# Performance work log

Hardware: AMD Instinct MI355X
Metric: run time of the kernel (lower is better)

## Reference

```python
import jax, jax.numpy as jnp
import numpy as np

Z_RES, N_RES = 128, 512
M_PTS = 2_000_000


def trilinear_devoxelize(grid, coords):
    """Gather-based trilinear interpolation.
    grid:   (Z, N, N, C) voxel grid
    coords: (M, 3) float positions in voxel index space (z, x, y)
    returns (M, C)
    """
    Zd, Nd = grid.shape[0], grid.shape[1]
    c0f = jnp.floor(coords)
    frac = coords - c0f                      # (M, 3) fractional offsets
    maxi = jnp.array([Zd - 1, Nd - 1, Nd - 1], dtype=jnp.int32)
    c0 = jnp.clip(c0f.astype(jnp.int32), 0, maxi)
    c1 = jnp.clip(c0 + 1, 0, maxi)
    fz, fx, fy = frac[:, 0:1], frac[:, 1:2], frac[:, 2:3]
    gz, gx, gy = 1.0 - fz, 1.0 - fx, 1.0 - fy

    def g(zi, xi, yi):
        return grid[zi, xi, yi]              # (M, C) gather

    out = (g(c0[:, 0], c0[:, 1], c0[:, 2]) * gz * gx * gy
         + g(c0[:, 0], c0[:, 1], c1[:, 2]) * gz * gx * fy
         + g(c0[:, 0], c1[:, 1], c0[:, 2]) * gz * fx * gy
         + g(c0[:, 0], c1[:, 1], c1[:, 2]) * gz * fx * fy
         + g(c1[:, 0], c0[:, 1], c0[:, 2]) * fz * gx * gy
         + g(c1[:, 0], c0[:, 1], c1[:, 2]) * fz * gx * fy
         + g(c1[:, 0], c1[:, 1], c0[:, 2]) * fz * fx * gy
         + g(c1[:, 0], c1[:, 1], c1[:, 2]) * fz * fx * fy)
    return out


def setup_inputs() -> dict:
    key = jax.random.key(0)
    k1, k2 = jax.random.split(key)
    extents = jnp.array([Z_RES - 1, N_RES - 1, N_RES - 1], jnp.float32)
    coords = jax.random.uniform(k1, (M_PTS, 3), dtype=jnp.float32) * extents
    # init_scale = 1.0 -> albedo ~ U[0,1); normal initialized to zeros (per module)
    albedo = jax.random.uniform(k2, (Z_RES, N_RES, N_RES), dtype=jnp.float32)
    normal = jnp.zeros((Z_RES, N_RES, N_RES, 3), dtype=jnp.float32)
    return {"coords": coords, "albedo": albedo, "normal": normal}


def reference(coords, albedo, normal):
    base_normal = jnp.array([-1.0, 0.0, 0.0], dtype=jnp.float32)
    a = trilinear_devoxelize(albedo[..., None], coords)[:, 0]   # (M,)
    n = trilinear_devoxelize(normal, coords)                    # (M, 3)
    a = jax.nn.elu(a)
    n = jnp.tanh(n) + base_normal
    # F.normalize(dim=1, eps=1e-12): divide by max(||n||, eps)
    norm = jnp.maximum(jnp.linalg.norm(n, axis=1, keepdims=True), 1e-12)
    n = n / norm
    return (a, n)
```

## Files before the change

### kernel.cpp

```cpp
#include <hip/hip_runtime.h>
#include <math.h>

#define ZR 128
#define NR 512
#define ZB1 4096

typedef unsigned int u32x4 __attribute__((ext_vector_type(4)));
typedef unsigned short u16x8 __attribute__((ext_vector_type(8)));
typedef unsigned long long u64x2v __attribute__((ext_vector_type(2)));


__device__ __forceinline__ float bf16_to_f32(unsigned short u) {
    return __uint_as_float(((unsigned int)u) << 16);
}

__device__ __forceinline__ unsigned short f32_to_bf16_rne(float v) {
    unsigned int u = __float_as_uint(v);
    return (unsigned short)((u + 0x7FFFu + ((u >> 16) & 1u)) >> 16);
}

__device__ __forceinline__ float extract_bf16(u64x2v v, int yo) {
    unsigned long long w = (yo & 4) ? v.y : v.x;
    unsigned int sh = ((unsigned)yo & 3u) << 4;
    return bf16_to_f32((unsigned short)(w >> sh));
}

__device__ __forceinline__ void zcheck_range(
    const u32x4* __restrict__ normal4, long long lo, long long hi,
    long long rank, long long nthreads, unsigned int* __restrict__ flag)
{
    unsigned int acc = 0;
    long long i = lo + rank * 256 + threadIdx.x;
    for (; i + nthreads < hi; i += 2 * nthreads) {
        u32x4 v0 = __builtin_nontemporal_load(&normal4[i]);
        u32x4 v1 = __builtin_nontemporal_load(&normal4[i + nthreads]);
        acc |= v0.x | v0.y | v0.z | v0.w | v1.x | v1.y | v1.z | v1.w;
    }
    if (i < hi) {
        u32x4 v = __builtin_nontemporal_load(&normal4[i]);
        acc |= v.x | v.y | v.z | v.w;
    }
    if (__ballot(acc != 0) && ((threadIdx.x & 63) == 0))
        atomicOr(flag, 1u);
}

__device__ __forceinline__ float interp_rows(
    const unsigned short* __restrict__ tiled,
    float cz, float cx, float cy)
{
    float fz0 = floorf(cz), fx0 = floorf(cx), fy0 = floorf(cy);
    float fz = cz - fz0, fx = cx - fx0, fy = cy - fy0;

    int z0 = min(max((int)fz0, 0), ZR - 1);
    int x0 = min(max((int)fx0, 0), NR - 1);
    int y0 = min(max((int)fy0, 0), NR - 1);
    int z1 = min(z0 + 1, ZR - 1);
    int x1 = min(x0 + 1, NR - 1);
    int y1 = min(y0 + 1, NR - 1);

    float gz = 1.0f - fz, gx = 1.0f - fx, gy = 1.0f - fy;

    float w000 = gz * gx * gy, w001 = gz * gx * fy;
    float w010 = gz * fx * gy, w011 = gz * fx * fy;
    float w100 = fz * gx * gy, w101 = fz * gx * fy;
    float w110 = fz * fx * gy, w111 = fz * fx * fy;

    int xo0 = (x0 & 3) << 3, xo1 = (x1 & 3) << 3;
    int yo0 = y0 & 7,        yo1 = y1 & 7;
    int c0 = (y0 >> 3) << 5, c1 = (y1 >> 3) << 5;
    int r00 = ((z0 << 7) + (x0 >> 2)) << 11;
    int r01 = ((z0 << 7) + (x1 >> 2)) << 11;
    int r10 = ((z1 << 7) + (x0 >> 2)) << 11;
    int r11 = ((z1 << 7) + (x1 >> 2)) << 11;

    const u64x2v* base = (const u64x2v*)tiled;

    u64x2v vA = base[(r00 + c0 + xo0) >> 3];
    u64x2v vB = base[(r01 + c0 + xo1) >> 3];
    u64x2v vC = base[(r10 + c0 + xo0) >> 3];
    u64x2v vD = base[(r11 + c0 + xo1) >> 3];

    u64x2v vA2 = vA, vB2 = vB, vC2 = vC, vD2 = vD;
    if (c1 != c0) {
        vA2 = base[(r00 + c1 + xo0) >> 3];
        vB2 = base[(r01 + c1 + xo1) >> 3];
        vC2 = base[(r10 + c1 + xo0) >> 3];
        vD2 = base[(r11 + c1 + xo1) >> 3];
    }

    return
        extract_bf16(vA,  yo0) * w000 + extract_bf16(vA2, yo1) * w001 +
        extract_bf16(vB,  yo0) * w010 + extract_bf16(vB2, yo1) * w011 +
        extract_bf16(vC,  yo0) * w100 + extract_bf16(vC2, yo1) * w101 +
        extract_bf16(vD,  yo0) * w110 + extract_bf16(vD2, yo1) * w111;
}

__global__ __launch_bounds__(256) void phase1_kernel(
    const float* __restrict__ albedo,
    unsigned short* __restrict__ tiled,
    const u32x4* __restrict__ normal4,
    const unsigned int* __restrict__ normal_tail, int tail_cnt,
    unsigned int* __restrict__ flag,
    float* __restrict__ out_n,
    long long n4, int M, int FB)
{
    unsigned int b = blockIdx.x;

    if (b < (unsigned)ZB1) {
        if (b == 0 && threadIdx.x < (unsigned)tail_cnt) {
            if (normal_tail[threadIdx.x]) atomicOr(flag, 1u);
        }
        zcheck_range(normal4, 0, n4, (long long)b, (long long)ZB1 * 256, flag);
        return;
    }
    b -= (unsigned)ZB1;

    if (b < 16384u) {
        int z = (int)(b >> 7);
        int xt = (int)(b & 127u);

        __shared__ float s[2048];
        const u32x4* src = (const u32x4*)(albedo + ((size_t)z * NR + (size_t)xt * 4) * NR);
        for (int k = threadIdx.x; k < 512; k += 256) {
            u32x4 v = __builtin_nontemporal_load(&src[k]);
            ((u32x4*)s)[k] = v;
        }
        __syncthreads();

        unsigned short* dst = tiled + (size_t)b * 2048;
        int t8 = threadIdx.x * 8;
        u16x8 outv;
#pragma unroll
        for (int j = 0; j < 8; j++) {
            int k = t8 + j;
            int yt = k >> 5;
            int r = k & 31;
            int xr = r >> 3;
            int yy = r & 7;
            outv[j] = f32_to_bf16_rne(s[xr * 512 + (yt << 3) + yy]);
        }
        *(u16x8*)(dst + t8) = outv;
        return;
    }
    b -= 16384u;

    long long total = 3LL * M;
    if ((M & 3) == 0) {
        long long f4 = (long long)b * 256 + threadIdx.x;
        long long nf4 = total >> 2;
        if (f4 < nf4) {
            const unsigned int B = 0xBF800000u;
            int rmod = (int)(f4 % 3);
            u32x4 v;
            if (rmod == 0)      v = (u32x4){B, 0u, 0u, B};
            else if (rmod == 1) v = (u32x4){0u, 0u, B, 0u};
            else                v = (u32x4){0u, B, 0u, 0u};
            __builtin_nontemporal_store(v, &((u32x4*)out_n)[f4]);
        }
    } else {
        long long stride = (long long)FB * 256;
        for (long long qq = (long long)b * 256 + threadIdx.x; qq < total; qq += stride)
            out_n[qq] = ((qq % 3) == 0) ? -1.0f : 0.0f;
    }
}

__global__ __launch_bounds__(256) void interp_kernel(
    const float* __restrict__ coords,
    const unsigned short* __restrict__ tiled,
    float* __restrict__ out_a,
    int M)
{
    int i = blockIdx.x * 256 + threadIdx.x;
    if (i >= M) return;

    float cz = coords[3 * i + 0];
    float cx = coords[3 * i + 1];
    float cy = coords[3 * i + 2];

    float a = interp_rows(tiled, cz, cx, cy);
    a = (a > 0.0f) ? a : expm1f(a);
    __builtin_nontemporal_store(a, &out_a[i]);
}

__global__ __launch_bounds__(256) void normal_full_kernel(
    const float* __restrict__ coords,
    const float* __restrict__ normal,
    const unsigned int* __restrict__ flag,
    float* __restrict__ out_n,
    int M)
{
    if (*flag == 0) return;

    int stride = gridDim.x * 256;
    for (int i = blockIdx.x * 256 + threadIdx.x; i < M; i += stride) {
        float cz = coords[3 * i + 0];
        float cx = coords[3 * i + 1];
        float cy = coords[3 * i + 2];

        float fz0 = floorf(cz), fx0 = floorf(cx), fy0 = floorf(cy);
        float fz = cz - fz0, fx = cx - fx0, fy = cy - fy0;

        int z0 = min(max((int)fz0, 0), ZR - 1);
        int x0 = min(max((int)fx0, 0), NR - 1);
        int y0 = min(max((int)fy0, 0), NR - 1);
        int z1 = min(z0 + 1, ZR - 1);
        int x1 = min(x0 + 1, NR - 1);
        int y1 = min(y0 + 1, NR - 1);

        float gz = 1.0f - fz, gx = 1.0f - fx, gy = 1.0f - fy;

        float w000 = gz * gx * gy, w001 = gz * gx * fy;
        float w010 = gz * fx * gy, w011 = gz * fx * fy;
        float w100 = fz * gx * gy, w101 = fz * gx * fy;
        float w110 = fz * fx * gy, w111 = fz * fx * fy;

        size_t b00 = ((size_t)z0 * NR + x0) * NR;
        size_t b01 = ((size_t)z0 * NR + x1) * NR;
        size_t b10 = ((size_t)z1 * NR + x0) * NR;
        size_t b11 = ((size_t)z1 * NR + x1) * NR;

        float n0 = 0.0f, n1 = 0.0f, n2 = 0.0f;
#define ACC(base, yy, w)                                           \
        {                                                          \
            const float* qp = normal + ((base) + (size_t)(yy)) * 3;\
            n0 += qp[0] * (w);                                     \
            n1 += qp[1] * (w);                                     \
            n2 += qp[2] * (w);                                     \
        }
        ACC(b00, y0, w000); ACC(b00, y1, w001);
        ACC(b01, y0, w010); ACC(b01, y1, w011);
        ACC(b10, y0, w100); ACC(b10, y1, w101);
        ACC(b11, y0, w110); ACC(b11, y1, w111);
#undef ACC

        n0 = tanhf(n0) - 1.0f;
        n1 = tanhf(n1);
        n2 = tanhf(n2);

        float nrm = sqrtf(n0 * n0 + n1 * n1 + n2 * n2);
        nrm = fmaxf(nrm, 1e-12f);
        float inv = 1.0f / nrm;

        out_n[3 * i + 0] = n0 * inv;
        out_n[3 * i + 1] = n1 * inv;
        out_n[3 * i + 2] = n2 * inv;
    }
}

__global__ __launch_bounds__(256) void devox_direct(
    const float* __restrict__ coords,
    const float* __restrict__ albedo,
    const float* __restrict__ normal,
    float* __restrict__ out_a,
    float* __restrict__ out_n,
    int M)
{
    int i = blockIdx.x * 256 + threadIdx.x;
    if (i >= M) return;

    float cz = coords[3 * i + 0];
    float cx = coords[3 * i + 1];
    float cy = coords[3 * i + 2];

    float fz0 = floorf(cz), fx0 = floorf(cx), fy0 = floorf(cy);
    float fz = cz - fz0, fx = cx - fx0, fy = cy - fy0;

    int z0 = min(max((int)fz0, 0), ZR - 1);
    int x0 = min(max((int)fx0, 0), NR - 1);
    int y0 = min(max((int)fy0, 0), NR - 1);
    int z1 = min(z0 + 1, ZR - 1);
    int x1 = min(x0 + 1, NR - 1);
    int y1 = min(y0 + 1, NR - 1);

    float gz = 1.0f - fz, gx = 1.0f - fx, gy = 1.0f - fy;
    float w000 = gz * gx * gy, w001 = gz * gx * fy;
    float w010 = gz * fx * gy, w011 = gz * fx * fy;
    float w100 = fz * gx * gy, w101 = fz * gx * fy;
    float w110 = fz * fx * gy, w111 = fz * fx * fy;

    size_t b00 = ((size_t)z0 * NR + x0) * NR;
    size_t b01 = ((size_t)z0 * NR + x1) * NR;
    size_t b10 = ((size_t)z1 * NR + x0) * NR;
    size_t b11 = ((size_t)z1 * NR + x1) * NR;

    float a =
        albedo[b00 + y0] * w000 + albedo[b00 + y1] * w001 +
        albedo[b01 + y0] * w010 + albedo[b01 + y1] * w011 +
        albedo[b10 + y0] * w100 + albedo[b10 + y1] * w101 +
        albedo[b11 + y0] * w110 + albedo[b11 + y1] * w111;

    float n0 = 0.0f, n1 = 0.0f, n2 = 0.0f;
#define ACC(base, yy, w)                                           \
    {                                                              \
        const float* qp = normal + ((base) + (size_t)(yy)) * 3;    \
        n0 += qp[0] * (w);                                         \
        n1 += qp[1] * (w);                                         \
        n2 += qp[2] * (w);                                         \
    }
    ACC(b00, y0, w000); ACC(b00, y1, w001);
    ACC(b01, y0, w010); ACC(b01, y1, w011);
    ACC(b10, y0, w100); ACC(b10, y1, w101);
    ACC(b11, y0, w110); ACC(b11, y1, w111);
#undef ACC

    a = (a > 0.0f) ? a : expm1f(a);
    n0 = tanhf(n0) - 1.0f;
    n1 = tanhf(n1);
    n2 = tanhf(n2);
    float nrm = sqrtf(n0 * n0 + n1 * n1 + n2 * n2);
    nrm = fmaxf(nrm, 1e-12f);
    float inv = 1.0f / nrm;

    out_a[i] = a;
    out_n[3 * i + 0] = n0 * inv;
    out_n[3 * i + 1] = n1 * inv;
    out_n[3 * i + 2] = n2 * inv;
}

extern "C" void kernel_launch(void* const* d_in, const int* in_sizes, int n_in,
                              void* d_out, int out_size, void* d_ws, size_t ws_size,
                              hipStream_t stream) {
    const float* coords = (const float*)d_in[0];
    const float* albedo = (const float*)d_in[1];
    const float* normal = (const float*)d_in[2];

    int M = in_sizes[0] / 3;
    long long normal_elems = (long long)in_sizes[2];
    long long n4 = normal_elems / 4;
    int tail_cnt = (int)(normal_elems & 3);
    const unsigned int* normal_tail = (const unsigned int*)normal + n4 * 4;

    float* out = (float*)d_out;
    float* out_a = out;
    float* out_n = out + M;

    size_t tiled_off = 256;
    size_t tiled_bytes = (size_t)128 * 128 * 64 * 32 * 2;
    if (ws_size < tiled_off + tiled_bytes) {
        int nblk = (M + 255) / 256;
        devox_direct<<<nblk, 256, 0, stream>>>(coords, albedo, normal, out_a, out_n, M);
        return;
    }

    unsigned int* flag = (unsigned int*)d_ws;
    unsigned short* tiled = (unsigned short*)((char*)d_ws + tiled_off);

    (void)hipMemsetAsync(flag, 0, sizeof(unsigned int), stream);

    long long total_n = 3LL * M;
    int FB = ((M & 3) == 0) ? (int)((total_n / 4 + 255) / 256) : 2048;
    if (FB < 1) FB = 1;
    phase1_kernel<<<ZB1 + 16384 + FB, 256, 0, stream>>>(
        albedo, tiled, (const u32x4*)normal, normal_tail, tail_cnt,
        flag, out_n, n4, M, FB);

    int iblk = (M + 255) / 256;
    interp_kernel<<<iblk, 256, 0, stream>>>(coords, tiled, out_a, M);

    normal_full_kernel<<<2048, 256, 0, stream>>>(coords, normal, flag, out_n, M);
}
```

Baseline: 681.8 us.

## Move normal zero-check into interp kernel and process two points per thread

The zero-scan of the normal grid moves out of the repack kernel and into the interpolation kernel, where every third block does zero-check work and the other two do interpolation. Mixing them lets the bandwidth-heavy scan overlap with the latency-bound gathers. Each interpolation thread now handles two points, using float2 coordinate loads and a paired output store. The risk is uneven block mixes and a different zcheck grid size changing scan efficiency.

```diff
diff --git a/kernel.cpp b/kernel.cpp
--- a/kernel.cpp
+++ b/kernel.cpp
@@ -3,11 +3,11 @@
 
 #define ZR 128
 #define NR 512
-#define ZB1 4096
 
 typedef unsigned int u32x4 __attribute__((ext_vector_type(4)));
 typedef unsigned short u16x8 __attribute__((ext_vector_type(8)));
 typedef unsigned long long u64x2v __attribute__((ext_vector_type(2)));
+typedef float f32x2 __attribute__((ext_vector_type(2)));
 
 
 __device__ __forceinline__ float bf16_to_f32(unsigned short u) {
@@ -95,25 +95,13 @@
         extract_bf16(vD,  yo0) * w110 + extract_bf16(vD2, yo1) * w111;
 }
 
-__global__ __launch_bounds__(256) void phase1_kernel(
+__global__ __launch_bounds__(256) void repack_fill_kernel(
     const float* __restrict__ albedo,
     unsigned short* __restrict__ tiled,
-    const u32x4* __restrict__ normal4,
-    const unsigned int* __restrict__ normal_tail, int tail_cnt,
-    unsigned int* __restrict__ flag,
     float* __restrict__ out_n,
-    long long n4, int M, int FB)
+    int M, int FB)
 {
     unsigned int b = blockIdx.x;
-
-    if (b < (unsigned)ZB1) {
-        if (b == 0 && threadIdx.x < (unsigned)tail_cnt) {
-            if (normal_tail[threadIdx.x]) atomicOr(flag, 1u);
-        }
-        zcheck_range(normal4, 0, n4, (long long)b, (long long)ZB1 * 256, flag);
-        return;
-    }
-    b -= (unsigned)ZB1;
 
     if (b < 16384u) {
         int z = (int)(b >> 7);
@@ -164,22 +152,46 @@
     }
 }
 
-__global__ __launch_bounds__(256) void interp_kernel(
+__global__ __launch_bounds__(256) void interp_zcheck_kernel(
     const float* __restrict__ coords,
     const unsigned short* __restrict__ tiled,
+    const u32x4* __restrict__ normal4,
+    const unsigned int* __restrict__ normal_tail, int tail_cnt,
+    unsigned int* __restrict__ flag,
     float* __restrict__ out_a,
-    int M)
-{
-    int i = blockIdx.x * 256 + threadIdx.x;
-    if (i >= M) return;
-
-    float cz = coords[3 * i + 0];
-    float cx = coords[3 * i + 1];
-    float cy = coords[3 * i + 2];
-
-    float a = interp_rows(tiled, cz, cx, cy);
-    a = (a > 0.0f) ? a : expm1f(a);
-    __builtin_nontemporal_store(a, &out_a[i]);
+    int M, long long n4, int ZB)
+{
+    unsigned int b = blockIdx.x;
+    unsigned int q = b / 3u;
+    unsigned int r = b - 3u * q;
+
+    if (r == 2u) {
+        if (q == 0 && threadIdx.x < (unsigned)tail_cnt) {
+            if (normal_tail[threadIdx.x]) atomicOr(flag, 1u);
+        }
+        zcheck_range(normal4, 0, n4, (long long)q, (long long)ZB * 256, flag);
+        return;
+    }
+
+    int ib = (int)(2u * q + r);
+    int t = ib * 256 + (int)threadIdx.x;
+    int i0 = t * 2;
+    if (i0 >= M) return;
+
+    const float2* cp = (const float2*)(coords + (size_t)i0 * 3);
+    float2 q0 = cp[0], q1 = cp[1], q2 = cp[2];
+
+    float a0 = interp_rows(tiled, q0.x, q0.y, q1.x);
+    a0 = (a0 > 0.0f) ? a0 : expm1f(a0);
+
+    if (i0 + 1 < M) {
+        float a1 = interp_rows(tiled, q1.y, q2.x, q2.y);
+        a1 = (a1 > 0.0f) ? a1 : expm1f(a1);
+        f32x2 av; av.x = a0; av.y = a1;
+        __builtin_nontemporal_store(av, (f32x2*)(out_a + i0));
+    } else {
+        out_a[i0] = a0;
+    }
 }
 
 __global__ __launch_bounds__(256) void normal_full_kernel(
@@ -350,12 +362,15 @@
     long long total_n = 3LL * M;
     int FB = ((M & 3) == 0) ? (int)((total_n / 4 + 255) / 256) : 2048;
     if (FB < 1) FB = 1;
-    phase1_kernel<<<ZB1 + 16384 + FB, 256, 0, stream>>>(
-        albedo, tiled, (const u32x4*)normal, normal_tail, tail_cnt,
-        flag, out_n, n4, M, FB);
-
-    int iblk = (M + 255) / 256;
-    interp_kernel<<<iblk, 256, 0, stream>>>(coords, tiled, out_a, M);
+    repack_fill_kernel<<<16384 + FB, 256, 0, stream>>>(albedo, tiled, out_n, M, FB);
+
+    int IB = (M + 511) / 512;
+    IB = (IB + 1) & ~1;
+    if (IB < 2) IB = 2;
+    int ZB = IB / 2;
+    interp_zcheck_kernel<<<3 * ZB, 256, 0, stream>>>(
+        coords, tiled, (const u32x4*)normal, normal_tail, tail_cnt,
+        flag, out_a, M, n4, ZB);
 
     normal_full_kernel<<<2048, 256, 0, stream>>>(coords, normal, flag, out_n, M);
 }
```

After: 674.5 us. About the same (-1.1%).

## Bin points into spatial cells and interpolate from shared-memory albedo tiles

Applied to the files above, without the earlier changes.

Replaces the bf16 retiling of the whole albedo grid plus per-point global gathers with a scatter pass that buckets points by spatial cell (4x32x32 voxels) using atomics. A per-cell kernel then loads a small albedo halo tile into LDS and interpolates every point in the bucket from shared memory, writing output by original index. Points beyond the per-cell capacity go to an overflow list handled by a separate global-gather kernel. This removes the full-grid bf16 conversion pass and the precision loss, at the cost of atomic contention, scattered output writes and an extra record write/read of the points.

```diff
diff --git a/kernel.cpp b/kernel.cpp
--- a/kernel.cpp
+++ b/kernel.cpp
@@ -3,27 +3,17 @@
 
 #define ZR 128
 #define NR 512
-#define ZB1 4096
+
+#define NCX 16
+#define NCY 16
+#define NCELL 8192
+#define CAP 512
+#define SLZ 5
+#define SLX 33
+#define SLY 33
+#define SVOL (SLZ * SLX * SLY)
 
 typedef unsigned int u32x4 __attribute__((ext_vector_type(4)));
-typedef unsigned short u16x8 __attribute__((ext_vector_type(8)));
-typedef unsigned long long u64x2v __attribute__((ext_vector_type(2)));
-
-
-__device__ __forceinline__ float bf16_to_f32(unsigned short u) {
-    return __uint_as_float(((unsigned int)u) << 16);
-}
-
-__device__ __forceinline__ unsigned short f32_to_bf16_rne(float v) {
-    unsigned int u = __float_as_uint(v);
-    return (unsigned short)((u + 0x7FFFu + ((u >> 16) & 1u)) >> 16);
-}
-
-__device__ __forceinline__ float extract_bf16(u64x2v v, int yo) {
-    unsigned long long w = (yo & 4) ? v.y : v.x;
-    unsigned int sh = ((unsigned)yo & 3u) << 4;
-    return bf16_to_f32((unsigned short)(w >> sh));
-}
 
 __device__ __forceinline__ void zcheck_range(
     const u32x4* __restrict__ normal4, long long lo, long long hi,
@@ -44,105 +34,54 @@
         atomicOr(flag, 1u);
 }
 
-__device__ __forceinline__ float interp_rows(
-    const unsigned short* __restrict__ tiled,
-    float cz, float cx, float cy)
-{
-    float fz0 = floorf(cz), fx0 = floorf(cx), fy0 = floorf(cy);
-    float fz = cz - fz0, fx = cx - fx0, fy = cy - fy0;
-
-    int z0 = min(max((int)fz0, 0), ZR - 1);
-    int x0 = min(max((int)fx0, 0), NR - 1);
-    int y0 = min(max((int)fy0, 0), NR - 1);
-    int z1 = min(z0 + 1, ZR - 1);
-    int x1 = min(x0 + 1, NR - 1);
-    int y1 = min(y0 + 1, NR - 1);
-
-    float gz = 1.0f - fz, gx = 1.0f - fx, gy = 1.0f - fy;
-
-    float w000 = gz * gx * gy, w001 = gz * gx * fy;
-    float w010 = gz * fx * gy, w011 = gz * fx * fy;
-    float w100 = fz * gx * gy, w101 = fz * gx * fy;
-    float w110 = fz * fx * gy, w111 = fz * fx * fy;
-
-    int xo0 = (x0 & 3) << 3, xo1 = (x1 & 3) << 3;
-    int yo0 = y0 & 7,        yo1 = y1 & 7;
-    int c0 = (y0 >> 3) << 5, c1 = (y1 >> 3) << 5;
-    int r00 = ((z0 << 7) + (x0 >> 2)) << 11;
-    int r01 = ((z0 << 7) + (x1 >> 2)) << 11;
-    int r10 = ((z1 << 7) + (x0 >> 2)) << 11;
-    int r11 = ((z1 << 7) + (x1 >> 2)) << 11;
-
-    const u64x2v* base = (const u64x2v*)tiled;
-
-    u64x2v vA = base[(r00 + c0 + xo0) >> 3];
-    u64x2v vB = base[(r01 + c0 + xo1) >> 3];
-    u64x2v vC = base[(r10 + c0 + xo0) >> 3];
-    u64x2v vD = base[(r11 + c0 + xo1) >> 3];
-
-    u64x2v vA2 = vA, vB2 = vB, vC2 = vC, vD2 = vD;
-    if (c1 != c0) {
-        vA2 = base[(r00 + c1 + xo0) >> 3];
-        vB2 = base[(r01 + c1 + xo1) >> 3];
-        vC2 = base[(r10 + c1 + xo0) >> 3];
-        vD2 = base[(r11 + c1 + xo1) >> 3];
-    }
-
-    return
-        extract_bf16(vA,  yo0) * w000 + extract_bf16(vA2, yo1) * w001 +
-        extract_bf16(vB,  yo0) * w010 + extract_bf16(vB2, yo1) * w011 +
-        extract_bf16(vC,  yo0) * w100 + extract_bf16(vC2, yo1) * w101 +
-        extract_bf16(vD,  yo0) * w110 + extract_bf16(vD2, yo1) * w111;
-}
-
-__global__ __launch_bounds__(256) void phase1_kernel(
-    const float* __restrict__ albedo,
-    unsigned short* __restrict__ tiled,
+__global__ __launch_bounds__(256) void scatter_zcheck_fill_kernel(
+    const float* __restrict__ coords,
     const u32x4* __restrict__ normal4,
     const unsigned int* __restrict__ normal_tail, int tail_cnt,
     unsigned int* __restrict__ flag,
+    unsigned int* __restrict__ cnt,
+    unsigned int* __restrict__ ovf_cnt,
+    float4* __restrict__ recs,
+    float4* __restrict__ ovf,
     float* __restrict__ out_n,
-    long long n4, int M, int FB)
+    int M, long long n4, int SB, int ZB, int FB)
 {
     unsigned int b = blockIdx.x;
 
-    if (b < (unsigned)ZB1) {
+    if (b < (unsigned)SB) {
+        int base = (int)b * 2048;
+#pragma unroll
+        for (int k = 0; k < 8; k++) {
+            int i = base + k * 256 + (int)threadIdx.x;
+            if (i >= M) break;
+            size_t o = 3 * (size_t)i;
+            float cz = coords[o], cx = coords[o + 1], cy = coords[o + 2];
+            int z0 = min(max((int)floorf(cz), 0), ZR - 1);
+            int x0 = min(max((int)floorf(cx), 0), NR - 1);
+            int y0 = min(max((int)floorf(cy), 0), NR - 1);
+            int cell = ((z0 >> 2) * NCX + (x0 >> 5)) * NCY + (y0 >> 5);
+            unsigned int slot = atomicAdd(&cnt[cell], 1u);
+            float4 r;
+            r.x = cz; r.y = cx; r.z = cy; r.w = __uint_as_float((unsigned int)i);
+            if (slot < CAP) {
+                recs[(size_t)cell * CAP + slot] = r;
+            } else {
+                unsigned int os = atomicAdd(ovf_cnt, 1u);
+                ovf[os] = r;
+            }
+        }
+        return;
+    }
+    b -= (unsigned)SB;
+
+    if (b < (unsigned)ZB) {
         if (b == 0 && threadIdx.x < (unsigned)tail_cnt) {
             if (normal_tail[threadIdx.x]) atomicOr(flag, 1u);
         }
-        zcheck_range(normal4, 0, n4, (long long)b, (long long)ZB1 * 256, flag);
+        zcheck_range(normal4, 0, n4, (long long)b, (long long)ZB * 256, flag);
         return;
     }
-    b -= (unsigned)ZB1;
-
-    if (b < 16384u) {
-        int z = (int)(b >> 7);
-        int xt = (int)(b & 127u);
-
-        __shared__ float s[2048];
-        const u32x4* src = (const u32x4*)(albedo + ((size_t)z * NR + (size_t)xt * 4) * NR);
-        for (int k = threadIdx.x; k < 512; k += 256) {
-            u32x4 v = __builtin_nontemporal_load(&src[k]);
-            ((u32x4*)s)[k] = v;
-        }
-        __syncthreads();
-
-        unsigned short* dst = tiled + (size_t)b * 2048;
-        int t8 = threadIdx.x * 8;
-        u16x8 outv;
-#pragma unroll
-        for (int j = 0; j < 8; j++) {
-            int k = t8 + j;
-            int yt = k >> 5;
-            int r = k & 31;
-            int xr = r >> 3;
-            int yy = r & 7;
-            outv[j] = f32_to_bf16_rne(s[xr * 512 + (yt << 3) + yy]);
-        }
-        *(u16x8*)(dst + t8) = outv;
-        return;
-    }
-    b -= 16384u;
+    b -= (unsigned)ZB;
 
     long long total = 3LL * M;
     if ((M & 3) == 0) {
@@ -164,22 +103,116 @@
     }
 }
 
-__global__ __launch_bounds__(256) void interp_kernel(
-    const float* __restrict__ coords,
-    const unsigned short* __restrict__ tiled,
+__global__ __launch_bounds__(256) void interp_cell_kernel(
+    const float* __restrict__ albedo,
+    const unsigned int* __restrict__ cnt,
+    const float4* __restrict__ recs,
+    float* __restrict__ out_a)
+{
+    __shared__ float s[SVOL];
+
+    int c = blockIdx.x;
+    int zc = c >> 8;
+    int xc = (c >> 4) & 15;
+    int yc = c & 15;
+    int Z = zc << 2, X = xc << 5, Y = yc << 5;
+
+    for (int i = threadIdx.x; i < SVOL; i += 256) {
+        int lz = i / (SLX * SLY);
+        int rem = i - lz * (SLX * SLY);
+        int lx = rem / SLY;
+        int ly = rem - lx * SLY;
+        int gz = min(Z + lz, ZR - 1);
+        int gx = min(X + lx, NR - 1);
+        int gy = min(Y + ly, NR - 1);
+        s[i] = albedo[((size_t)gz * NR + gx) * NR + gy];
+    }
+    __syncthreads();
+
+    int np = min((int)cnt[c], CAP);
+    const float4* rbase = recs + (size_t)c * CAP;
+
+    for (int p = threadIdx.x; p < np; p += 256) {
+        float4 r = rbase[p];
+        float cz = r.x, cx = r.y, cy = r.z;
+        unsigned int idx = __float_as_uint(r.w);
+
+        float fz0 = floorf(cz), fx0 = floorf(cx), fy0 = floorf(cy);
+        float fz = cz - fz0, fx = cx - fx0, fy = cy - fy0;
+
+        int z0 = min(max((int)fz0, 0), ZR - 1);
+        int x0 = min(max((int)fx0, 0), NR - 1);
+        int y0 = min(max((int)fy0, 0), NR - 1);
+
+        float gz = 1.0f - fz, gx = 1.0f - fx, gy = 1.0f - fy;
+        float w000 = gz * gx * gy, w001 = gz * gx * fy;
+        float w010 = gz * fx * gy, w011 = gz * fx * fy;
+        float w100 = fz * gx * gy, w101 = fz * gx * fy;
+        float w110 = fz * fx * gy, w111 = fz * fx * fy;
+
+        int lz0 = z0 - Z, lx0 = x0 - X, ly0 = y0 - Y;
+        int b00 = lz0 * (SLX * SLY) + lx0 * SLY + ly0;
+        int b01 = b00 + SLY;
+        int b10 = b00 + (SLX * SLY);
+        int b11 = b10 + SLY;
+
+        float a =
+            s[b00] * w000 + s[b00 + 1] * w001 +
+            s[b01] * w010 + s[b01 + 1] * w011 +
+            s[b10] * w100 + s[b10 + 1] * w101 +
+            s[b11] * w110 + s[b11 + 1] * w111;
+
+        a = (a > 0.0f) ? a : expm1f(a);
+        out_a[idx] = a;
+    }
+}
+
+__global__ __launch_bounds__(256) void overflow_kernel(
+    const float4* __restrict__ ovf,
+    const unsigned int* __restrict__ ovf_cnt,
+    const float* __restrict__ albedo,
     float* __restrict__ out_a,
     int M)
 {
-    int i = blockIdx.x * 256 + threadIdx.x;
-    if (i >= M) return;
-
-    float cz = coords[3 * i + 0];
-    float cx = coords[3 * i + 1];
-    float cy = coords[3 * i + 2];
-
-    float a = interp_rows(tiled, cz, cx, cy);
-    a = (a > 0.0f) ? a : expm1f(a);
-    __builtin_nontemporal_store(a, &out_a[i]);
+    int n = (int)*ovf_cnt;
+    if (n <= 0) return;
+    if (n > M) n = M;
+    int stride = gridDim.x * 256;
+    for (int p = blockIdx.x * 256 + threadIdx.x; p < n; p += stride) {
+        float4 r = ovf[p];
+        float cz = r.x, cx = r.y, cy = r.z;
+        unsigned int idx = __float_as_uint(r.w);
+
+        float fz0 = floorf(cz), fx0 = floorf(cx), fy0 = floorf(cy);
+        float fz = cz - fz0, fx = cx - fx0, fy = cy - fy0;
+
+        int z0 = min(max((int)fz0, 0), ZR - 1);
+        int x0 = min(max((int)fx0, 0), NR - 1);
+        int y0 = min(max((int)fy0, 0), NR - 1);
+        int z1 = min(z0 + 1, ZR - 1);
+        int x1 = min(x0 + 1, NR - 1);
+        int y1 = min(y0 + 1, NR - 1);
+
+        float gz = 1.0f - fz, gx = 1.0f - fx, gy = 1.0f - fy;
+        float w000 = gz * gx * gy, w001 = gz * gx * fy;
+        float w010 = gz * fx * gy, w011 = gz * fx * fy;
+        float w100 = fz * gx * gy, w101 = fz * gx * fy;
+        float w110 = fz * fx * gy, w111 = fz * fx * fy;
+
+        size_t b00 = ((size_t)z0 * NR + x0) * NR;
+        size_t b01 = ((size_t)z0 * NR + x1) * NR;
+        size_t b10 = ((size_t)z1 * NR + x0) * NR;
+        size_t b11 = ((size_t)z1 * NR + x1) * NR;
+
+        float a =
+            albedo[b00 + y0] * w000 + albedo[b00 + y1] * w001 +
+            albedo[b01 + y0] * w010 + albedo[b01 + y1] * w011 +
+            albedo[b10 + y0] * w100 + albedo[b10 + y1] * w101 +
+            albedo[b11 + y0] * w110 + albedo[b11 + y1] * w111;
+
+        a = (a > 0.0f) ? a : expm1f(a);
+        out_a[idx] = a;
+    }
 }
 
 __global__ __launch_bounds__(256) void normal_full_kernel(
@@ -334,28 +367,38 @@
     float* out_a = out;
     float* out_n = out + M;
 
-    size_t tiled_off = 256;
-    size_t tiled_bytes = (size_t)128 * 128 * 64 * 32 * 2;
-    if (ws_size < tiled_off + tiled_bytes) {
+    size_t cnt_off = 4096;
+    size_t rec_off = 65536;
+    size_t rec_bytes = (size_t)NCELL * CAP * 16;
+    size_t ovf_off = rec_off + rec_bytes;
+    size_t ovf_bytes = (size_t)M * 16;
+    if (ws_size < ovf_off + ovf_bytes) {
         int nblk = (M + 255) / 256;
         devox_direct<<<nblk, 256, 0, stream>>>(coords, albedo, normal, out_a, out_n, M);
         return;
     }
 
     unsigned int* flag = (unsigned int*)d_ws;
-    unsigned short* tiled = (unsigned short*)((char*)d_ws + tiled_off);
-
-    (void)hipMemsetAsync(flag, 0, sizeof(unsigned int), stream);
-
+    unsigned int* ovf_cnt = (unsigned int*)((char*)d_ws + 64);
+    unsigned int* cnt = (unsigned int*)((char*)d_ws + cnt_off);
+    float4* recs = (float4*)((char*)d_ws + rec_off);
+    float4* ovf = (float4*)((char*)d_ws + ovf_off);
+
+    (void)hipMemsetAsync(d_ws, 0, cnt_off + (size_t)NCELL * 4, stream);
+
+    int SB = (M + 2047) / 2048;
+    if (SB < 1) SB = 1;
+    int ZB = 3072;
     long long total_n = 3LL * M;
     int FB = ((M & 3) == 0) ? (int)((total_n / 4 + 255) / 256) : 2048;
     if (FB < 1) FB = 1;
-    phase1_kernel<<<ZB1 + 16384 + FB, 256, 0, stream>>>(
-        albedo, tiled, (const u32x4*)normal, normal_tail, tail_cnt,
-        flag, out_n, n4, M, FB);
-
-    int iblk = (M + 255) / 256;
-    interp_kernel<<<iblk, 256, 0, stream>>>(coords, tiled, out_a, M);
+    scatter_zcheck_fill_kernel<<<SB + ZB + FB, 256, 0, stream>>>(
+        coords, (const u32x4*)normal, normal_tail, tail_cnt,
+        flag, cnt, ovf_cnt, recs, ovf, out_n, M, n4, SB, ZB, FB);
+
+    interp_cell_kernel<<<NCELL, 256, 0, stream>>>(albedo, cnt, recs, out_a);
+
+    overflow_kernel<<<256, 256, 0, stream>>>(ovf, ovf_cnt, albedo, out_a, M);
 
     normal_full_kernel<<<2048, 256, 0, stream>>>(coords, normal, flag, out_n, M);
 }
```

New measurement: 716.7 us. +5.1%, slower.
